# Kernel optimization log

Hardware: AMD Instinct MI355X
Metric: run time of the kernel (lower is better)

Reference implementation:

```python
import jax, jax.numpy as jnp
import numpy as np

B, C, H, W = 8, 320, 32, 32
HEADS, DHEAD = 8, 40
CTX_LEN, CTX_DIM = 77, 768
FF_INNER = 4 * C
GROUPS = 32
HW = H * W


def setup_inputs() -> dict:
    key = jax.random.key(0)
    ks = jax.random.split(key, 16)
    def nrm(k, shape, s=0.02):
        return (jax.random.normal(k, shape) * s).astype(jnp.float32)
    z = lambda *s: jnp.zeros(s, jnp.float32)
    o = lambda *s: jnp.ones(s, jnp.float32)
    inp = {}
    inp["x"] = jax.random.normal(ks[0], (B, C, H, W), jnp.float32)
    inp["context"] = jax.random.normal(ks[1], (B, CTX_LEN, CTX_DIM), jnp.float32)
    inp["vis_mask"] = jax.random.uniform(ks[2], (B, HW, HW)) > 0.5
    inp["v2t_mask"] = jax.random.uniform(ks[3], (B, HW, CTX_LEN)) > 0.5
    inp["gn_scale"] = o(C); inp["gn_bias"] = z(C)
    inp["proj_in_w"] = nrm(ks[4], (C, C)); inp["proj_in_b"] = z(C)
    inp["n1_s"] = o(C); inp["n1_b"] = z(C)
    inp["wq1"] = nrm(ks[5], (C, C)); inp["wk1"] = nrm(ks[6], (C, C)); inp["wv1"] = nrm(ks[7], (C, C))
    inp["wo1"] = nrm(ks[8], (C, C)); inp["bo1"] = z(C)
    inp["n2_s"] = o(C); inp["n2_b"] = z(C)
    inp["wq2"] = nrm(ks[9], (C, C)); inp["wk2"] = nrm(ks[10], (CTX_DIM, C)); inp["wv2"] = nrm(ks[11], (CTX_DIM, C))
    inp["wo2"] = nrm(ks[12], (C, C)); inp["bo2"] = z(C)
    inp["n3_s"] = o(C); inp["n3_b"] = z(C)
    inp["ff_w1"] = nrm(ks[13], (C, 2 * FF_INNER)); inp["ff_b1"] = z(2 * FF_INNER)
    inp["ff_w2"] = nrm(ks[14], (FF_INNER, C)); inp["ff_b2"] = z(C)
    inp["proj_out_w"] = nrm(ks[15], (C, C)); inp["proj_out_b"] = z(C)
    return inp


def group_norm(x, scale, bias, eps=1e-6):
    b, c, h, w = x.shape
    xg = x.reshape(b, GROUPS, -1)
    mu = xg.mean(-1, keepdims=True)
    var = xg.var(-1, keepdims=True)
    xn = ((xg - mu) * jax.lax.rsqrt(var + eps)).reshape(b, c, h, w)
    return xn * scale[None, :, None, None] + bias[None, :, None, None]


def layer_norm(x, s, b, eps=1e-5):
    mu = x.mean(-1, keepdims=True)
    var = x.var(-1, keepdims=True)
    return (x - mu) * jax.lax.rsqrt(var + eps) * s + b


def mha(xq, ctx, wq, wk, wv, wo, bo, mask):
    # CrossAttention: manual einsum softmax with boolean mask broadcast over heads
    b, n, _ = xq.shape
    m = ctx.shape[1]
    split = lambda t: t.reshape(b, -1, HEADS, DHEAD).transpose(0, 2, 1, 3)
    q = split(xq @ wq)   # [b,h,n,d]
    k = split(ctx @ wk)  # [b,h,m,d]
    v = split(ctx @ wv)
    sim = jnp.einsum('bhid,bhjd->bhij', q, k) * (DHEAD ** -0.5)
    if mask is not None:
        sim = jnp.where(mask[:, None, :, :], sim, jnp.finfo(sim.dtype).min)
    attn = jax.nn.softmax(sim, axis=-1)
    out = jnp.einsum('bhij,bhjd->bhid', attn, v)
    out = out.transpose(0, 2, 1, 3).reshape(b, n, HEADS * DHEAD)
    return out @ wo + bo


def reference(x, context, vis_mask, v2t_mask, gn_scale, gn_bias, proj_in_w, proj_in_b,
              n1_s, n1_b, wq1, wk1, wv1, wo1, bo1,
              n2_s, n2_b, wq2, wk2, wv2, wo2, bo2,
              n3_s, n3_b, ff_w1, ff_b1, ff_w2, ff_b2,
              proj_out_w, proj_out_b):
    x_in = x
    h = group_norm(x, gn_scale, gn_bias)
    # 1x1 conv proj_in == per-pixel linear; flatten b c h w -> b (hw) c
    h = h.reshape(B, C, HW).transpose(0, 2, 1) @ proj_in_w + proj_in_b
    # masked self-attention (vis mask)
    h = h + mha(layer_norm(h, n1_s, n1_b), layer_norm(h, n1_s, n1_b),
                wq1, wk1, wv1, wo1, bo1, vis_mask)
    # masked cross-attention to text (v2t mask)
    h = h + mha(layer_norm(h, n2_s, n2_b), context,
                wq2, wk2, wv2, wo2, bo2, v2t_mask)
    # GEGLU feedforward (glu=True, mult=4)
    y = layer_norm(h, n3_s, n3_b) @ ff_w1 + ff_b1
    a, g = jnp.split(y, 2, axis=-1)
    h = h + (a * jax.nn.gelu(g, approximate=False)) @ ff_w2 + ff_b2
    # proj_out + residual
    out = (h @ proj_out_w + proj_out_b).transpose(0, 2, 1).reshape(B, C, H, W)
    return out + x_in
```

## Files before the change

kernel.cpp:

```cpp
#include <hip/hip_runtime.h>
#include <hip/hip_bf16.h>
#include <math.h>


#define Bsz   8
#define Cch   320
#define HW    1024
#define NTOK  (Bsz*HW)
#define HEADS 8
#define DHEAD 40
#define CTXL  77
#define CTXD  768
#define FFI   1280
#define MCTX  (Bsz*CTXL)
#define MCTXP 640

typedef unsigned short u16;
typedef unsigned long long u64;
typedef __attribute__((ext_vector_type(8))) u16    u16x8;
typedef __attribute__((ext_vector_type(8))) __bf16 bf16x8;
typedef __attribute__((ext_vector_type(4))) float  f32x4;

__device__ inline u16 f2b(float f) {
    unsigned u = __float_as_uint(f);
    return (u16)((u + 0x7FFFu + ((u >> 16) & 1u)) >> 16);
}

__global__ __launch_bounds__(256) void gn_apply(
    const float* __restrict__ x, const float* __restrict__ gnA,
    const float* __restrict__ gnB, u16* __restrict__ out)
{
    __shared__ u16 T[64*72];
    const int tid = threadIdx.x;
    const int c0 = blockIdx.x * 64;
    const int p0 = blockIdx.y * 64;
    const int b  = blockIdx.z;
    for (int e = tid; e < 512; e += 256) {
        int r = e >> 3, ch = e & 7;
        const float* src = x + ((size_t)(b*Cch + c0 + r))*HW + p0 + ch*8;
        float a  = gnA[b*Cch + c0 + r];
        float bb = gnB[b*Cch + c0 + r];
        float4 v0 = *(const float4*)src;
        float4 v1 = *(const float4*)(src + 4);
        u16x8 val;
        val[0] = f2b(v0.x*a + bb); val[1] = f2b(v0.y*a + bb);
        val[2] = f2b(v0.z*a + bb); val[3] = f2b(v0.w*a + bb);
        val[4] = f2b(v1.x*a + bb); val[5] = f2b(v1.y*a + bb);
        val[6] = f2b(v1.z*a + bb); val[7] = f2b(v1.w*a + bb);
        *(u16x8*)&T[r*72 + (ch ^ (r & 7))*8] = val;
    }
    __syncthreads();
    for (int e = tid; e < 4096; e += 256) {
        int p = e >> 6, c = e & 63;
        u16 v = T[c*72 + (((p >> 3) ^ (c & 7))*8) + (p & 7)];
        out[((size_t)(b*HW + p0 + p))*Cch + c0 + c] = v;
    }
}

__global__ __launch_bounds__(256) void layernorm_kernel(
    const float* __restrict__ in, const float* __restrict__ s,
    const float* __restrict__ bgain, u16* __restrict__ out)
{
    int t = blockIdx.x*4 + (threadIdx.x >> 6);
    int lane = threadIdx.x & 63;
    const float* row = in + (size_t)t*Cch;
    float v[5];
    float sum = 0.f, sq = 0.f;
    #pragma unroll
    for (int i = 0; i < 5; ++i) {
        v[i] = row[lane + 64*i];
        sum += v[i]; sq += v[i]*v[i];
    }
    #pragma unroll
    for (int off = 32; off > 0; off >>= 1) {
        sum += __shfl_xor(sum, off);
        sq  += __shfl_xor(sq,  off);
    }
    float mean = sum * (1.f/320.f);
    float var  = sq  * (1.f/320.f) - mean*mean;
    float inv  = rsqrtf(var + 1e-5f);
    u16* orow = out + (size_t)t*Cch;
    #pragma unroll
    for (int i = 0; i < 5; ++i) {
        int c = lane + 64*i;
        orow[c] = f2b((v[i]-mean)*inv*s[c] + bgain[c]);
    }
}

struct WDesc { const float* src; u16* dst; int K; int N; int tiles; float scl; };
struct WPack { WDesc w[12]; };

#define WT_TILES 620
#define CTXBLK   240

__global__ __launch_bounds__(256) void preamble(
    WPack p, const float* __restrict__ ctxsrc, u16* __restrict__ ctxdst,
    const void* __restrict__ vis, const void* __restrict__ v2t,
    u64* __restrict__ bvis, u64* __restrict__ bv2t,
    const float* __restrict__ x, const float* __restrict__ gscale,
    const float* __restrict__ gbias, float* __restrict__ gnA,
    float* __restrict__ gnB)
{
    __shared__ u16 T[64*72];
    int blk = blockIdx.x;
    int tid = threadIdx.x;
    if (blk < WT_TILES) {
        int t = blk;
        #pragma unroll
        for (int i = 0; i < 12; ++i) {
            int nt = p.w[i].tiles;
            if (t < nt) {
                const int K = p.w[i].K, N = p.w[i].N;
                const int ntN = N >> 6;
                const int tk = t / ntN, tn = t - tk*ntN;
                const float scl = p.w[i].scl;
                const float* src = p.w[i].src;
                u16* dst = p.w[i].dst;
                for (int e = tid; e < 512; e += 256) {
                    int r = e >> 3, ch = e & 7;
                    const float* sp = src + (size_t)(tk*64 + r)*N + tn*64 + ch*8;
                    float4 v0 = *(const float4*)sp;
                    float4 v1 = *(const float4*)(sp + 4);
                    u16x8 val;
                    val[0] = f2b(v0.x*scl); val[1] = f2b(v0.y*scl);
                    val[2] = f2b(v0.z*scl); val[3] = f2b(v0.w*scl);
                    val[4] = f2b(v1.x*scl); val[5] = f2b(v1.y*scl);
                    val[6] = f2b(v1.z*scl); val[7] = f2b(v1.w*scl);
                    *(u16x8*)&T[r*72 + (ch ^ (r & 7))*8] = val;
                }
                __syncthreads();
                for (int e = tid; e < 4096; e += 256) {
                    int n = e >> 6, k = e & 63;
                    u16 v = T[k*72 + (((n >> 3) ^ (k & 7))*8) + (n & 7)];
                    dst[(size_t)(tn*64 + n)*K + tk*64 + k] = v;
                }
                return;
            }
            t -= nt;
        }
        return;
    }
    if (blk < WT_TILES + CTXBLK) {
        int idx = (blk - WT_TILES)*2048 + tid*8;
        int r = idx / CTXD;
        u16x8 val = {};
        if (r < MCTX) {
            float4 v0 = *(const float4*)(ctxsrc + idx);
            float4 v1 = *(const float4*)(ctxsrc + idx + 4);
            val[0] = f2b(v0.x); val[1] = f2b(v0.y);
            val[2] = f2b(v0.z); val[3] = f2b(v0.w);
            val[4] = f2b(v1.x); val[5] = f2b(v1.y);
            val[6] = f2b(v1.z); val[7] = f2b(v1.w);
        }
        *(u16x8*)(ctxdst + idx) = val;
        return;
    }
    if (blk >= WT_TILES + CTXBLK + 4096) {
        int gb = blk - (WT_TILES + CTXBLK + 4096);
        int b = gb >> 5, g = gb & 31;
        __shared__ float rs[256], rq[256];
        const float4* xg = (const float4*)(x + ((size_t)b*Cch + g*10)*HW);
        float s = 0.f, q = 0.f;
        #pragma unroll
        for (int i = 0; i < 10; ++i) {
            float4 v = xg[tid + i*256];
            s += v.x + v.y + v.z + v.w;
            q += v.x*v.x + v.y*v.y + v.z*v.z + v.w*v.w;
        }
        rs[tid] = s; rq[tid] = q; __syncthreads();
        for (int off = 128; off > 0; off >>= 1) {
            if (tid < off) { rs[tid] += rs[tid+off]; rq[tid] += rq[tid+off]; }
            __syncthreads();
        }
        if (tid < 10) {
            float mean = rs[0] * (1.f/10240.f);
            float var  = rq[0] * (1.f/10240.f) - mean*mean;
            float inv  = rsqrtf(var + 1e-6f);
            int chn = g*10 + tid;
            float a = inv * gscale[chn];
            gnA[b*Cch + chn] = a;
            gnB[b*Cch + chn] = gbias[chn] - mean*a;
        }
        return;
    }
    __shared__ int any;
    if (tid == 0) any = 0;
    __syncthreads();
    const unsigned char* probe = (const unsigned char*)vis;
    for (int i = tid; i < 4096; i += 256)
        if ((i & 3) && probe[i]) any = 1;
    __syncthreads();
    const int isU8 = any;
    int mb = blk - WT_TILES - CTXBLK;
    const void* mask; u64* bits; int Lkv, nw;
    if (mb < 2048) { mask = vis; bits = bvis; Lkv = HW;   nw = 16; }
    else           { mask = v2t; bits = bv2t; Lkv = CTXL; nw = 2; mb -= 2048; }
    const int wv = tid >> 6, lane = tid & 63;
    const int row = mb*4 + wv;
    const unsigned char* m8  = (const unsigned char*)mask;
    const int*           m32 = (const int*)mask;
    const size_t base = (size_t)row * Lkv;
    for (int w = 0; w < nw; ++w) {
        int j = w*64 + lane;
        bool on = (j < Lkv) && (isU8 ? (m8[base+j] != 0) : (m32[base+j] != 0));
        u64 word = __ballot(on);
        if (lane == 0) bits[(size_t)row*nw + w] = word;
    }
}

__global__ __launch_bounds__(512) void gemm_bf16(
    const u16* __restrict__ A, const u16* __restrict__ Wt,
    const float* __restrict__ bias, const float* __restrict__ res,
    float* __restrict__ out, u16* __restrict__ out_bf, int M, int N, int K)
{
    __shared__ u16 As[2][128*40];
    __shared__ u16 Bs[2][64*40];
    const int tid  = threadIdx.x;
    const int lane = tid & 63;
    const int w    = tid >> 6;
    const int mp   = w >> 1;
    const int np   = w & 1;
    const int m0   = blockIdx.y * 128;
    const int n0   = blockIdx.x * 64;
    const int fr   = lane & 15, fg = lane >> 4;
    const int ar   = tid >> 2, ac = tid & 3;
    const bool hasB = tid < 256;

    const u16* pa = A  + (size_t)(m0 + ar)*K + ac*8;
    const u16* pb = Wt + (size_t)(n0 + ar)*K + ac*8;
    const int nk = K >> 5;

    *(u16x8*)&As[0][ar*40 + ac*8] = *(const u16x8*)pa;
    if (hasB) *(u16x8*)&Bs[0][ar*40 + ac*8] = *(const u16x8*)pb;
    u16x8 xa = *(const u16x8*)(pa + 32);
    u16x8 ya = *(const u16x8*)(pa + 64);
    u16x8 xb = {}, yb = {};
    if (hasB) { xb = *(const u16x8*)(pb + 32); yb = *(const u16x8*)(pb + 64); }

    f32x4 acc[2][2] = {};
    for (int i = 0; i < nk; i += 2) {
        __syncthreads();
        *(u16x8*)&As[1][ar*40 + ac*8] = xa;
        if (hasB) *(u16x8*)&Bs[1][ar*40 + ac*8] = xb;
        if (i + 3 < nk) {
            xa = *(const u16x8*)(pa + 32*(i+3));
            if (hasB) xb = *(const u16x8*)(pb + 32*(i+3));
        }
        {
            bf16x8 a0 = *(const bf16x8*)&As[0][(mp*32      + fr)*40 + fg*8];
            bf16x8 a1 = *(const bf16x8*)&As[0][(mp*32 + 16 + fr)*40 + fg*8];
            #pragma unroll
            for (int t = 0; t < 2; ++t) {
                bf16x8 b = *(const bf16x8*)&Bs[0][((np*2+t)*16 + fr)*40 + fg*8];
                acc[0][t] = __builtin_amdgcn_mfma_f32_16x16x32_bf16(a0, b, acc[0][t], 0, 0, 0);
                acc[1][t] = __builtin_amdgcn_mfma_f32_16x16x32_bf16(a1, b, acc[1][t], 0, 0, 0);
            }
        }
        __syncthreads();
        if (i + 2 < nk) {
            *(u16x8*)&As[0][ar*40 + ac*8] = ya;
            if (hasB) *(u16x8*)&Bs[0][ar*40 + ac*8] = yb;
            if (i + 4 < nk) {
                ya = *(const u16x8*)(pa + 32*(i+4));
                if (hasB) yb = *(const u16x8*)(pb + 32*(i+4));
            }
        }
        {
            bf16x8 a0 = *(const bf16x8*)&As[1][(mp*32      + fr)*40 + fg*8];
            bf16x8 a1 = *(const bf16x8*)&As[1][(mp*32 + 16 + fr)*40 + fg*8];
            #pragma unroll
            for (int t = 0; t < 2; ++t) {
                bf16x8 b = *(const bf16x8*)&Bs[1][((np*2+t)*16 + fr)*40 + fg*8];
                acc[0][t] = __builtin_amdgcn_mfma_f32_16x16x32_bf16(a0, b, acc[0][t], 0, 0, 0);
                acc[1][t] = __builtin_amdgcn_mfma_f32_16x16x32_bf16(a1, b, acc[1][t], 0, 0, 0);
            }
        }
    }
    #pragma unroll
    for (int at = 0; at < 2; ++at) {
        #pragma unroll
        for (int t = 0; t < 2; ++t) {
            int gn = n0 + (np*2+t)*16 + fr;
            float bv = bias ? bias[gn] : 0.f;
            #pragma unroll
            for (int i = 0; i < 4; ++i) {
                int gm = m0 + mp*32 + at*16 + fg*4 + i;
                float v = acc[at][t][i] + bv;
                if (res) v += res[(size_t)gm*N + gn];
                if (out) out[(size_t)gm*N + gn] = v;
                if (out_bf) out_bf[(size_t)gm*N + gn] = f2b(v);
            }
        }
    }
}

__global__ __launch_bounds__(512) void gemm_pout(
    const u16* __restrict__ A, const u16* __restrict__ Wt,
    const float* __restrict__ bias, const float* __restrict__ x,
    float* __restrict__ out, int K)
{
    __shared__ u16 As[2][128*40];
    __shared__ u16 Bs[2][64*40];
    const int tid  = threadIdx.x;
    const int lane = tid & 63;
    const int w    = tid >> 6;
    const int mp   = w >> 1;
    const int np   = w & 1;
    const int m0   = blockIdx.y * 128;
    const int n0   = blockIdx.x * 64;
    const int fr   = lane & 15, fg = lane >> 4;
    const int ar   = tid >> 2, ac = tid & 3;
    const bool hasB = tid < 256;

    const u16* pa = A  + (size_t)(m0 + ar)*K + ac*8;
    const u16* pb = Wt + (size_t)(n0 + ar)*K + ac*8;
    const int nk = K >> 5;

    *(u16x8*)&As[0][ar*40 + ac*8] = *(const u16x8*)pa;
    if (hasB) *(u16x8*)&Bs[0][ar*40 + ac*8] = *(const u16x8*)pb;
    u16x8 xa = *(const u16x8*)(pa + 32);
    u16x8 ya = *(const u16x8*)(pa + 64);
    u16x8 xb = {}, yb = {};
    if (hasB) { xb = *(const u16x8*)(pb + 32); yb = *(const u16x8*)(pb + 64); }

    f32x4 acc[2][2] = {};
    for (int i = 0; i < nk; i += 2) {
        __syncthreads();
        *(u16x8*)&As[1][ar*40 + ac*8] = xa;
        if (hasB) *(u16x8*)&Bs[1][ar*40 + ac*8] = xb;
        if (i + 3 < nk) {
            xa = *(const u16x8*)(pa + 32*(i+3));
            if (hasB) xb = *(const u16x8*)(pb + 32*(i+3));
        }
        {
            bf16x8 a0 = *(const bf16x8*)&As[0][(mp*32      + fr)*40 + fg*8];
            bf16x8 a1 = *(const bf16x8*)&As[0][(mp*32 + 16 + fr)*40 + fg*8];
            #pragma unroll
            for (int t = 0; t < 2; ++t) {
                bf16x8 b = *(const bf16x8*)&Bs[0][((np*2+t)*16 + fr)*40 + fg*8];
                acc[0][t] = __builtin_amdgcn_mfma_f32_16x16x32_bf16(a0, b, acc[0][t], 0, 0, 0);
                acc[1][t] = __builtin_amdgcn_mfma_f32_16x16x32_bf16(a1, b, acc[1][t], 0, 0, 0);
            }
        }
        __syncthreads();
        if (i + 2 < nk) {
            *(u16x8*)&As[0][ar*40 + ac*8] = ya;
            if (hasB) *(u16x8*)&Bs[0][ar*40 + ac*8] = yb;
            if (i + 4 < nk) {
                ya = *(const u16x8*)(pa + 32*(i+4));
                if (hasB) yb = *(const u16x8*)(pb + 32*(i+4));
            }
        }
        {
            bf16x8 a0 = *(const bf16x8*)&As[1][(mp*32      + fr)*40 + fg*8];
            bf16x8 a1 = *(const bf16x8*)&As[1][(mp*32 + 16 + fr)*40 + fg*8];
            #pragma unroll
            for (int t = 0; t < 2; ++t) {
                bf16x8 b = *(const bf16x8*)&Bs[1][((np*2+t)*16 + fr)*40 + fg*8];
                acc[0][t] = __builtin_amdgcn_mfma_f32_16x16x32_bf16(a0, b, acc[0][t], 0, 0, 0);
                acc[1][t] = __builtin_amdgcn_mfma_f32_16x16x32_bf16(a1, b, acc[1][t], 0, 0, 0);
            }
        }
    }
    #pragma unroll
    for (int at = 0; at < 2; ++at) {
        #pragma unroll
        for (int t = 0; t < 2; ++t) {
            int gn = n0 + (np*2+t)*16 + fr;
            float bv = bias[gn];
            int gm0 = m0 + mp*32 + at*16 + fg*4;
            int b   = gm0 >> 10;
            int pcol= gm0 & (HW-1);
            size_t o = ((size_t)(b*Cch + gn))*HW + pcol;
            f32x4 xv = *(const f32x4*)&x[o];
            f32x4 vv;
            #pragma unroll
            for (int i = 0; i < 4; ++i) vv[i] = acc[at][t][i] + bv + xv[i];
            *(f32x4*)&out[o] = vv;
        }
    }
}

__global__ __launch_bounds__(512) void ctx_kv_gemm(
    const u16* __restrict__ ctx, const u16* __restrict__ wk,
    const u16* __restrict__ wv, u16* __restrict__ kout, u16* __restrict__ vout)
{
    __shared__ u16 As[2][64*40];
    __shared__ u16 Bs[2][64*40];
    const int tid  = threadIdx.x;
    const int lane = tid & 63;
    const int w    = tid >> 6;
    const int mg   = w >> 1;
    const int np   = w & 1;
    const int m0   = blockIdx.y * 64;
    const int n0   = blockIdx.x * 64;
    const u16* Wt  = blockIdx.z ? wv : wk;
    u16* outp      = blockIdx.z ? vout : kout;
    const int fr   = lane & 15, fg = lane >> 4;
    const bool isA = tid < 256;
    const int cr   = (tid & 255) >> 2, cc = tid & 3;

    const u16* ps = isA ? ctx + (size_t)(m0 + cr)*CTXD + cc*8
                        : Wt  + (size_t)(n0 + cr)*CTXD + cc*8;
    u16* s0 = isA ? &As[0][cr*40 + cc*8] : &Bs[0][cr*40 + cc*8];
    u16* s1 = isA ? &As[1][cr*40 + cc*8] : &Bs[1][cr*40 + cc*8];
    const int nk = CTXD >> 5;

    *(u16x8*)s0 = *(const u16x8*)ps;
    u16x8 xv = *(const u16x8*)(ps + 32);
    u16x8 yv = *(const u16x8*)(ps + 64);

    f32x4 acc[2] = {};
    for (int i = 0; i < nk; i += 2) {
        __syncthreads();
        *(u16x8*)s1 = xv;
        if (i + 3 < nk) xv = *(const u16x8*)(ps + 32*(i+3));
        {
            bf16x8 a = *(const bf16x8*)&As[0][(mg*16 + fr)*40 + fg*8];
            #pragma unroll
            for (int t = 0; t < 2; ++t) {
                bf16x8 b = *(const bf16x8*)&Bs[0][((np*2+t)*16 + fr)*40 + fg*8];
                acc[t] = __builtin_amdgcn_mfma_f32_16x16x32_bf16(a, b, acc[t], 0, 0, 0);
            }
        }
        __syncthreads();
        if (i + 2 < nk) {
            *(u16x8*)s0 = yv;
            if (i + 4 < nk) yv = *(const u16x8*)(ps + 32*(i+4));
        }
        {
            bf16x8 a = *(const bf16x8*)&As[1][(mg*16 + fr)*40 + fg*8];
            #pragma unroll
            for (int t = 0; t < 2; ++t) {
                bf16x8 b = *(const bf16x8*)&Bs[1][((np*2+t)*16 + fr)*40 + fg*8];
                acc[t] = __builtin_amdgcn_mfma_f32_16x16x32_bf16(a, b, acc[t], 0, 0, 0);
            }
        }
    }
    #pragma unroll
    for (int t = 0; t < 2; ++t) {
        int gn = n0 + (np*2+t)*16 + fr;
        #pragma unroll
        for (int i = 0; i < 4; ++i) {
            int gm = m0 + mg*16 + fg*4 + i;
            if (gm < MCTX)
                outp[(size_t)gm*Cch + gn] = f2b(acc[t][i]);
        }
    }
}

__global__ __launch_bounds__(256) void geglu_bf16(
    const u16* __restrict__ A, const u16* __restrict__ Wt,
    const float* __restrict__ b1, u16* __restrict__ out, int M, int K)
{
    __shared__ u16 As[2][128*40];
    __shared__ u16 Ba[2][64*40];
    __shared__ u16 Bg[2][64*40];
    const int tid  = threadIdx.x;
    const int lane = tid & 63;
    const int w    = tid >> 6;
    const int m0   = blockIdx.y * 128;
    const int n0   = blockIdx.x * 64;
    const int fr   = lane & 15, fg = lane >> 4;
    const int ar   = tid >> 2, ac = tid & 3;

    const u16* pa0 = A  + (size_t)(m0 + ar)*K      + ac*8;
    const u16* pa1 = A  + (size_t)(m0 + ar + 64)*K + ac*8;
    const u16* pba = Wt + (size_t)(n0 + ar)*K       + ac*8;
    const u16* pbg = Wt + (size_t)(FFI + n0 + ar)*K + ac*8;
    const int nk = K >> 5;

    *(u16x8*)&As[0][ar*40 + ac*8]      = *(const u16x8*)pa0;
    *(u16x8*)&As[0][(ar+64)*40 + ac*8] = *(const u16x8*)pa1;
    *(u16x8*)&Ba[0][ar*40 + ac*8]      = *(const u16x8*)pba;
    *(u16x8*)&Bg[0][ar*40 + ac*8]      = *(const u16x8*)pbg;
    u16x8 xa0 = *(const u16x8*)(pa0 + 32);
    u16x8 xa1 = *(const u16x8*)(pa1 + 32);
    u16x8 xba = *(const u16x8*)(pba + 32);
    u16x8 xbg = *(const u16x8*)(pbg + 32);
    u16x8 ya0 = *(const u16x8*)(pa0 + 64);
    u16x8 ya1 = *(const u16x8*)(pa1 + 64);
    u16x8 yba = *(const u16x8*)(pba + 64);
    u16x8 ybg = *(const u16x8*)(pbg + 64);

    f32x4 aca[2][4] = {}, acg[2][4] = {};
    for (int i = 0; i < nk; i += 2) {
        __syncthreads();
        *(u16x8*)&As[1][ar*40 + ac*8]      = xa0;
        *(u16x8*)&As[1][(ar+64)*40 + ac*8] = xa1;
        *(u16x8*)&Ba[1][ar*40 + ac*8]      = xba;
        *(u16x8*)&Bg[1][ar*40 + ac*8]      = xbg;
        if (i + 3 < nk) {
            xa0 = *(const u16x8*)(pa0 + 32*(i+3));
            xa1 = *(const u16x8*)(pa1 + 32*(i+3));
            xba = *(const u16x8*)(pba + 32*(i+3));
            xbg = *(const u16x8*)(pbg + 32*(i+3));
        }
        {
            bf16x8 a0 = *(const bf16x8*)&As[0][(w*32      + fr)*40 + fg*8];
            bf16x8 a1 = *(const bf16x8*)&As[0][(w*32 + 16 + fr)*40 + fg*8];
            #pragma unroll
            for (int nt = 0; nt < 4; ++nt) {
                bf16x8 ba = *(const bf16x8*)&Ba[0][(nt*16 + fr)*40 + fg*8];
                bf16x8 bg = *(const bf16x8*)&Bg[0][(nt*16 + fr)*40 + fg*8];
                aca[0][nt] = __builtin_amdgcn_mfma_f32_16x16x32_bf16(a0, ba, aca[0][nt], 0, 0, 0);
                aca[1][nt] = __builtin_amdgcn_mfma_f32_16x16x32_bf16(a1, ba, aca[1][nt], 0, 0, 0);
                acg[0][nt] = __builtin_amdgcn_mfma_f32_16x16x32_bf16(a0, bg, acg[0][nt], 0, 0, 0);
                acg[1][nt] = __builtin_amdgcn_mfma_f32_16x16x32_bf16(a1, bg, acg[1][nt], 0, 0, 0);
            }
        }
        __syncthreads();
        if (i + 2 < nk) {
            *(u16x8*)&As[0][ar*40 + ac*8]      = ya0;
            *(u16x8*)&As[0][(ar+64)*40 + ac*8] = ya1;
            *(u16x8*)&Ba[0][ar*40 + ac*8]      = yba;
            *(u16x8*)&Bg[0][ar*40 + ac*8]      = ybg;
            if (i + 4 < nk) {
                ya0 = *(const u16x8*)(pa0 + 32*(i+4));
                ya1 = *(const u16x8*)(pa1 + 32*(i+4));
                yba = *(const u16x8*)(pba + 32*(i+4));
                ybg = *(const u16x8*)(pbg + 32*(i+4));
            }
        }
        {
            bf16x8 a0 = *(const bf16x8*)&As[1][(w*32      + fr)*40 + fg*8];
            bf16x8 a1 = *(const bf16x8*)&As[1][(w*32 + 16 + fr)*40 + fg*8];
            #pragma unroll
            for (int nt = 0; nt < 4; ++nt) {
                bf16x8 ba = *(const bf16x8*)&Ba[1][(nt*16 + fr)*40 + fg*8];
                bf16x8 bg = *(const bf16x8*)&Bg[1][(nt*16 + fr)*40 + fg*8];
                aca[0][nt] = __builtin_amdgcn_mfma_f32_16x16x32_bf16(a0, ba, aca[0][nt], 0, 0, 0);
                aca[1][nt] = __builtin_amdgcn_mfma_f32_16x16x32_bf16(a1, ba, aca[1][nt], 0, 0, 0);
                acg[0][nt] = __builtin_amdgcn_mfma_f32_16x16x32_bf16(a0, bg, acg[0][nt], 0, 0, 0);
                acg[1][nt] = __builtin_amdgcn_mfma_f32_16x16x32_bf16(a1, bg, acg[1][nt], 0, 0, 0);
            }
        }
    }
    #pragma unroll
    for (int at = 0; at < 2; ++at) {
        #pragma unroll
        for (int nt = 0; nt < 4; ++nt) {
            int gn = n0 + nt*16 + fr;
            float ba = b1[gn], bg = b1[FFI + gn];
            #pragma unroll
            for (int i = 0; i < 4; ++i) {
                int gm = m0 + w*32 + at*16 + fg*4 + i;
                float av = aca[at][nt][i] + ba;
                float gv = acg[at][nt][i] + bg;
                float gel = 0.5f*gv*(1.f + erff(gv*0.70710678118654752f));
                out[(size_t)gm*FFI + gn] = f2b(av*gel);
            }
        }
    }
}

__global__ __launch_bounds__(256) void transpose_v(
    const u16* __restrict__ in, int istride, u16* __restrict__ out,
    int Ltok, int ostride)
{
    __shared__ u16 T[64*72];
    const int tid = threadIdx.x;
    const int c0 = blockIdx.x * 64;
    const int t0 = blockIdx.y * 64;
    const int b  = blockIdx.z;
    for (int e = tid; e < 512; e += 256) {
        int r = e >> 3, ch = e & 7;
        u16x8 val = {};
        if (t0 + r < Ltok)
            val = *(const u16x8*)(in + ((size_t)(b*Ltok + t0 + r))*istride + c0 + ch*8);
        *(u16x8*)&T[r*72 + (ch ^ (r & 7))*8] = val;
    }
    __syncthreads();
    for (int e = tid; e < 4096; e += 256) {
        int c = e >> 6, t = e & 63;
        u16 v = T[t*72 + (((c >> 3) ^ (t & 7))*8) + (c & 7)];
        out[((size_t)(b*Cch + c0 + c))*ostride + t0 + t] = v;
    }
}

__global__ __launch_bounds__(256) void flash_mfma(
    const u16* __restrict__ qb, int qstride,
    const u16* __restrict__ kb, int kstride,
    const u16* __restrict__ vt, int vstride,
    const u64* __restrict__ mbits, int nw,
    u16* __restrict__ out,
    int Lkv)
{
    __shared__ u16 QPs[64*72];
    __shared__ u16 Ks[64*72];
    __shared__ u16 Vs[48*72];

    const int tid  = threadIdx.x;
    const int lane = tid & 63;
    const int w    = tid >> 6;
    const int col  = lane & 15;
    const int quad = lane >> 4;
    const int q0   = blockIdx.x * 64;
    const int h    = blockIdx.y;
    const int b    = blockIdx.z;
    const int ch   = tid & 7;
    const int r0   = tid >> 3;

    {
        const u16* qT = qb + ((size_t)(b*HW + q0))*qstride + (size_t)h*DHEAD + ch*8;
        u16x8 v0 = {}, v1 = {};
        if (ch < 5) {
            v0 = *(const u16x8*)(qT + (size_t)r0*qstride);
            v1 = *(const u16x8*)(qT + (size_t)(r0+32)*qstride);
        }
        *(u16x8*)&QPs[r0*72 + ch*8]      = v0;
        *(u16x8*)&QPs[(r0+32)*72 + ch*8] = v1;
    }
    __syncthreads();
    const bf16x8 qa0 = *(const bf16x8*)&QPs[(w*16 + col)*72 +  0 + quad*8];
    const bf16x8 qa1 = *(const bf16x8*)&QPs[(w*16 + col)*72 + 32 + quad*8];

    const bool kok = ch < 5;
    const u16* kR0 = kb + (size_t)b*Lkv*kstride + (size_t)h*DHEAD + ch*8
                        + (size_t)r0*kstride;
    const u16* kR1 = kR0 + (size_t)32*kstride;
    const int d1   = 32 + (tid >> 3);
    const u16* vR0 = vt + ((size_t)(b*Cch + h*DHEAD))*vstride + ch*8
                        + (size_t)r0*vstride;
    const u16* vR1 = vt + ((size_t)(b*Cch + h*DHEAD))*vstride + ch*8
                        + (size_t)d1*vstride;
    const u64* mrow = mbits + ((size_t)(b*HW + q0 + w*16 + quad*4))*nw;

    f32x4 acc_o[3] = {};

    const int nkt = (Lkv + 63) / 64;
    for (int jt = 0; jt < nkt; ++jt) {
        const int j0 = jt*64;
        __syncthreads();
        {
            u16x8 v0 = {}, v1 = {};
            if (kok && (j0 + r0      < Lkv)) v0 = *(const u16x8*)kR0;
            if (kok && (j0 + r0 + 32 < Lkv)) v1 = *(const u16x8*)kR1;
            *(u16x8*)&Ks[r0*72 + ch*8]      = v0;
            *(u16x8*)&Ks[(r0+32)*72 + ch*8] = v1;
        }
        {
            u16x8 v0 = {};
            if (r0 < DHEAD) v0 = *(const u16x8*)vR0;
            *(u16x8*)&Vs[r0*72 + ch*8] = v0;
            if (tid < 128) {
                u16x8 v1 = {};
                if (d1 < DHEAD) v1 = *(const u16x8*)vR1;
                else if (d1 == DHEAD) {
                    #pragma unroll
                    for (int z = 0; z < 8; ++z) v1[z] = 0x3F80;
                }
                *(u16x8*)&Vs[d1*72 + ch*8] = v1;
            }
        }
        __syncthreads();

        u64 mw[4];
        #pragma unroll
        for (int i = 0; i < 4; ++i) mw[i] = mrow[i*nw + jt];

        f32x4 s[4] = {};
        #pragma unroll
        for (int nt = 0; nt < 4; ++nt) {
            bf16x8 b0 = *(const bf16x8*)&Ks[(nt*16 + col)*72 +  0 + quad*8];
            bf16x8 b1 = *(const bf16x8*)&Ks[(nt*16 + col)*72 + 32 + quad*8];
            s[nt] = __builtin_amdgcn_mfma_f32_16x16x32_bf16(qa0, b0, s[nt], 0, 0, 0);
            s[nt] = __builtin_amdgcn_mfma_f32_16x16x32_bf16(qa1, b1, s[nt], 0, 0, 0);
        }

        #pragma unroll
        for (int i = 0; i < 4; ++i) {
            #pragma unroll
            for (int nt = 0; nt < 4; ++nt) {
                float p = __builtin_amdgcn_exp2f(s[nt][i]);
                unsigned bits = (unsigned)(mw[i] >> (nt*16));
                s[nt][i] = ((bits >> col) & 1u) ? p : 0.f;
            }
        }

        #pragma unroll
        for (int nt = 0; nt < 4; ++nt)
            #pragma unroll
            for (int i = 0; i < 4; ++i)
                QPs[(w*16 + quad*4 + i)*68 + nt*16 + col] =
                    (u16)(__float_as_uint(s[nt][i]) >> 16);

        bf16x8 pa0, pa1;
        __builtin_memcpy(&pa0, &QPs[(w*16 + col)*68 +  0 + quad*8], 16);
        __builtin_memcpy(&pa1, &QPs[(w*16 + col)*68 + 32 + quad*8], 16);
        #pragma unroll
        for (int nt = 0; nt < 3; ++nt) {
            bf16x8 vb0 = *(const bf16x8*)&Vs[(nt*16 + col)*72 +  0 + quad*8];
            bf16x8 vb1 = *(const bf16x8*)&Vs[(nt*16 + col)*72 + 32 + quad*8];
            acc_o[nt] = __builtin_amdgcn_mfma_f32_16x16x32_bf16(pa0, vb0, acc_o[nt], 0, 0, 0);
            acc_o[nt] = __builtin_amdgcn_mfma_f32_16x16x32_bf16(pa1, vb1, acc_o[nt], 0, 0, 0);
        }

        kR0 += (size_t)64*kstride;
        kR1 += (size_t)64*kstride;
        vR0 += 64;
        vR1 += 64;
    }

    float inv_l[4];
    #pragma unroll
    for (int i = 0; i < 4; ++i)
        inv_l[i] = 1.f / __shfl(acc_o[2][i], (lane & 48) | 8);

    #pragma unroll
    for (int nt = 0; nt < 3; ++nt) {
        int d = nt*16 + col;
        if (d < DHEAD) {
            #pragma unroll
            for (int i = 0; i < 4; ++i) {
                int q = q0 + w*16 + quad*4 + i;
                out[((size_t)(b*HW + q))*Cch + h*DHEAD + d] = f2b(acc_o[nt][i] * inv_l[i]);
            }
        }
    }
}

extern "C" void kernel_launch(void* const* d_in, const int* in_sizes, int n_in,
                              void* d_out, int out_size, void* d_ws, size_t ws_size,
                              hipStream_t stream)
{
    const float* x        = (const float*)d_in[0];
    const float* context  = (const float*)d_in[1];
    const void*  vis_mask = d_in[2];
    const void*  v2t_mask = d_in[3];
    const float* gn_s     = (const float*)d_in[4];
    const float* gn_b     = (const float*)d_in[5];
    const float* proj_in_w= (const float*)d_in[6];
    const float* proj_in_b= (const float*)d_in[7];
    const float* n1_s     = (const float*)d_in[8];
    const float* n1_b     = (const float*)d_in[9];
    const float* wq1      = (const float*)d_in[10];
    const float* wk1      = (const float*)d_in[11];
    const float* wv1      = (const float*)d_in[12];
    const float* wo1      = (const float*)d_in[13];
    const float* bo1      = (const float*)d_in[14];
    const float* n2_s     = (const float*)d_in[15];
    const float* n2_b     = (const float*)d_in[16];
    const float* wq2      = (const float*)d_in[17];
    const float* wk2      = (const float*)d_in[18];
    const float* wv2      = (const float*)d_in[19];
    const float* wo2      = (const float*)d_in[20];
    const float* bo2      = (const float*)d_in[21];
    const float* n3_s     = (const float*)d_in[22];
    const float* n3_b     = (const float*)d_in[23];
    const float* ff_w1    = (const float*)d_in[24];
    const float* ff_b1    = (const float*)d_in[25];
    const float* ff_w2    = (const float*)d_in[26];
    const float* ff_b2    = (const float*)d_in[27];
    const float* pout_w   = (const float*)d_in[28];
    const float* pout_b   = (const float*)d_in[29];
    float* out = (float*)d_out;

    const size_t TOKC = (size_t)NTOK*Cch;
    float* ws   = (float*)d_ws;
    float* Hb   = ws;
    u16*   QKV  = (u16*)(Hb + TOKC);
    u16*   Vt_g = QKV + 3*TOKC;
    u16*   G_bf = QKV;
    u16*   T0b  = Vt_g + TOKC;
    u16*   T1b  = T0b + TOKC;
    u16*   Hb_bf= T1b + TOKC;
    u16*   Wbf  = Hb_bf + TOKC;
    u64*   mb_vis = (u64*)(Wbf + 2539520);
    u64*   mb_v2t = mb_vis + 131072;
    u16*   ctx_bf = (u16*)(mb_v2t + 16384);
    u16*   Kc_bf  = ctx_bf + MCTXP*CTXD;
    u16*   Vc_bf  = Kc_bf + 640*Cch;
    float* gnA    = (float*)(Vc_bf + 640*Cch);
    float* gnB    = gnA + Bsz*Cch;

    u16* w_q1  = Wbf;
    u16* w_k1  = Wbf +  102400;
    u16* w_v1  = Wbf +  204800;
    u16* w_pin = Wbf +  307200;
    u16* w_o1  = Wbf +  409600;
    u16* w_q2  = Wbf +  512000;
    u16* w_o2  = Wbf +  614400;
    u16* w_ff1 = Wbf +  716800;
    u16* w_ff2 = Wbf + 1536000;
    u16* w_po  = Wbf + 1945600;
    u16* w_k2  = Wbf + 2048000;
    u16* w_v2  = Wbf + 2293760;

    const float qscale = 0.15811388300841897f * 1.4426950408889634f;
    WPack pack;
    pack.w[0]  = { wq1,       w_q1,  Cch, Cch, 25,  qscale };
    pack.w[1]  = { wk1,       w_k1,  Cch, Cch, 25,  1.f };
    pack.w[2]  = { wv1,       w_v1,  Cch, Cch, 25,  1.f };
    pack.w[3]  = { proj_in_w, w_pin, Cch, Cch, 25,  1.f };
    pack.w[4]  = { wo1,       w_o1,  Cch, Cch, 25,  1.f };
    pack.w[5]  = { wq2,       w_q2,  Cch, Cch, 25,  qscale };
    pack.w[6]  = { wo2,       w_o2,  Cch, Cch, 25,  1.f };
    pack.w[7]  = { ff_w1,     w_ff1, Cch, 2*FFI, 200, 1.f };
    pack.w[8]  = { ff_w2,     w_ff2, FFI, Cch, 100, 1.f };
    pack.w[9]  = { pout_w,    w_po,  Cch, Cch, 25,  1.f };
    pack.w[10] = { wk2,       w_k2,  CTXD, Cch, 60, 1.f };
    pack.w[11] = { wv2,       w_v2,  CTXD, Cch, 60, 1.f };

    dim3 blk256(256);
    dim3 blk512(512);
    dim3 gTok(Cch/64, NTOK/128);
    dim3 gQKV(960/64, NTOK/128);
    dim3 gKV(Cch/64, MCTXP/64, 2);
    dim3 gFF(FFI/64, NTOK/128);
    dim3 gFA(HW/64, HEADS, Bsz);
    dim3 gTrS(Cch/64, HW/64, Bsz);
    dim3 gTrX(Cch/64, 2, Bsz);
    dim3 gGN(Cch/64, HW/64, Bsz);

    preamble<<<WT_TILES + CTXBLK + 4096 + 256, blk256, 0, stream>>>(
        pack, context, ctx_bf, vis_mask, v2t_mask, mb_vis, mb_v2t,
        x, gn_s, gn_b, gnA, gnB);

    gn_apply<<<gGN, blk256, 0, stream>>>(x, gnA, gnB, T0b);
    gemm_bf16<<<gTok, blk512, 0, stream>>>(T0b, w_pin, proj_in_b, nullptr, Hb, nullptr, NTOK, Cch, Cch);

    layernorm_kernel<<<NTOK/4, blk256, 0, stream>>>(Hb, n1_s, n1_b, T0b);
    gemm_bf16<<<gQKV, blk512, 0, stream>>>(T0b, w_q1, nullptr, nullptr, nullptr, QKV, NTOK, 960, Cch);
    transpose_v<<<gTrS, blk256, 0, stream>>>(QKV + 640, 960, Vt_g, HW, HW);
    flash_mfma<<<gFA, blk256, 0, stream>>>(QKV, 960, QKV + 320, 960, Vt_g, HW,
                                           mb_vis, 16, T1b, HW);
    gemm_bf16<<<gTok, blk512, 0, stream>>>(T1b, w_o1, bo1, Hb, Hb, nullptr, NTOK, Cch, Cch);

    layernorm_kernel<<<NTOK/4, blk256, 0, stream>>>(Hb, n2_s, n2_b, T0b);
    gemm_bf16<<<gTok, blk512, 0, stream>>>(T0b, w_q2, nullptr, nullptr, nullptr, QKV, NTOK, Cch, Cch);
    ctx_kv_gemm<<<gKV, blk512, 0, stream>>>(ctx_bf, w_k2, w_v2, Kc_bf, Vc_bf);
    transpose_v<<<gTrX, blk256, 0, stream>>>(Vc_bf, Cch, Vt_g, CTXL, 128);
    flash_mfma<<<gFA, blk256, 0, stream>>>(QKV, Cch, Kc_bf, Cch, Vt_g, 128,
                                           mb_v2t, 2, T1b, CTXL);
    gemm_bf16<<<gTok, blk512, 0, stream>>>(T1b, w_o2, bo2, Hb, Hb, nullptr, NTOK, Cch, Cch);

    layernorm_kernel<<<NTOK/4, blk256, 0, stream>>>(Hb, n3_s, n3_b, T0b);
    geglu_bf16<<<gFF, blk256, 0, stream>>>(T0b, w_ff1, ff_b1, G_bf, NTOK, Cch);
    gemm_bf16<<<gTok, blk512, 0, stream>>>(G_bf, w_ff2, ff_b2, Hb, nullptr, Hb_bf, NTOK, Cch, FFI);

    gemm_pout<<<gTok, blk512, 0, stream>>>(Hb_bf, w_po, pout_b, x, out, Cch);
}
```

Before: 387.9 us.

## Widen GEGLU kernel to 512 threads and prefetch K/V tiles in flash attention

The GEGLU GEMM now launches 512 threads per block. Each thread loads one A row chunk and one B row chunk, and the 8 waves are split into a 4x2 grid over M and N, so each wave holds half as many accumulators. The flash attention kernel now register-prefetches the next K/V tile from global memory while computing the current one, and writes the constant ones/zero rows of the V tile once instead of every iteration. The aim is more waves in flight and global-load latency hidden behind MFMA work. The cost is extra register pressure for the prefetch buffers, and the V-padding rows rely on staying untouched across iterations.

```diff
diff --git a/kernel.cpp b/kernel.cpp
--- a/kernel.cpp
+++ b/kernel.cpp
@@ -449,7 +449,7 @@
     }
 }
 
-__global__ __launch_bounds__(256) void geglu_bf16(
+__global__ __launch_bounds__(512) void geglu_bf16(
     const u16* __restrict__ A, const u16* __restrict__ Wt,
     const float* __restrict__ b1, u16* __restrict__ out, int M, int K)
 {
@@ -459,94 +459,83 @@
     const int tid  = threadIdx.x;
     const int lane = tid & 63;
     const int w    = tid >> 6;
+    const int mp   = w >> 1;
+    const int np   = w & 1;
     const int m0   = blockIdx.y * 128;
     const int n0   = blockIdx.x * 64;
     const int fr   = lane & 15, fg = lane >> 4;
     const int ar   = tid >> 2, ac = tid & 3;
-
-    const u16* pa0 = A  + (size_t)(m0 + ar)*K      + ac*8;
-    const u16* pa1 = A  + (size_t)(m0 + ar + 64)*K + ac*8;
-    const u16* pba = Wt + (size_t)(n0 + ar)*K       + ac*8;
-    const u16* pbg = Wt + (size_t)(FFI + n0 + ar)*K + ac*8;
-    const int nk = K >> 5;
-
-    *(u16x8*)&As[0][ar*40 + ac*8]      = *(const u16x8*)pa0;
-    *(u16x8*)&As[0][(ar+64)*40 + ac*8] = *(const u16x8*)pa1;
-    *(u16x8*)&Ba[0][ar*40 + ac*8]      = *(const u16x8*)pba;
-    *(u16x8*)&Bg[0][ar*40 + ac*8]      = *(const u16x8*)pbg;
-    u16x8 xa0 = *(const u16x8*)(pa0 + 32);
-    u16x8 xa1 = *(const u16x8*)(pa1 + 32);
-    u16x8 xba = *(const u16x8*)(pba + 32);
-    u16x8 xbg = *(const u16x8*)(pbg + 32);
-    u16x8 ya0 = *(const u16x8*)(pa0 + 64);
-    u16x8 ya1 = *(const u16x8*)(pa1 + 64);
-    u16x8 yba = *(const u16x8*)(pba + 64);
-    u16x8 ybg = *(const u16x8*)(pbg + 64);
-
-    f32x4 aca[2][4] = {}, acg[2][4] = {};
+    const int nk   = K >> 5;
+
+    const u16* pa = A + (size_t)(m0 + ar)*K + ac*8;
+    const int bq = (ar < 64) ? (n0 + ar) : (FFI + n0 + ar - 64);
+    const u16* pb = Wt + (size_t)bq*K + ac*8;
+    u16* bs0 = (ar < 64) ? &Ba[0][ar*40 + ac*8] : &Bg[0][(ar-64)*40 + ac*8];
+    u16* bs1 = (ar < 64) ? &Ba[1][ar*40 + ac*8] : &Bg[1][(ar-64)*40 + ac*8];
+
+    *(u16x8*)&As[0][ar*40 + ac*8] = *(const u16x8*)pa;
+    *(u16x8*)bs0 = *(const u16x8*)pb;
+    u16x8 xa = *(const u16x8*)(pa + 32);
+    u16x8 xb = *(const u16x8*)(pb + 32);
+    u16x8 ya = *(const u16x8*)(pa + 64);
+    u16x8 yb = *(const u16x8*)(pb + 64);
+
+    f32x4 aca[2][2] = {}, acg[2][2] = {};
     for (int i = 0; i < nk; i += 2) {
         __syncthreads();
-        *(u16x8*)&As[1][ar*40 + ac*8]      = xa0;
-        *(u16x8*)&As[1][(ar+64)*40 + ac*8] = xa1;
-        *(u16x8*)&Ba[1][ar*40 + ac*8]      = xba;
-        *(u16x8*)&Bg[1][ar*40 + ac*8]      = xbg;
+        *(u16x8*)&As[1][ar*40 + ac*8] = xa;
+        *(u16x8*)bs1 = xb;
         if (i + 3 < nk) {
-            xa0 = *(const u16x8*)(pa0 + 32*(i+3));
-            xa1 = *(const u16x8*)(pa1 + 32*(i+3));
-            xba = *(const u16x8*)(pba + 32*(i+3));
-            xbg = *(const u16x8*)(pbg + 32*(i+3));
+            xa = *(const u16x8*)(pa + 32*(i+3));
+            xb = *(const u16x8*)(pb + 32*(i+3));
         }
         {
-            bf16x8 a0 = *(const bf16x8*)&As[0][(w*32      + fr)*40 + fg*8];
-            bf16x8 a1 = *(const bf16x8*)&As[0][(w*32 + 16 + fr)*40 + fg*8];
-            #pragma unroll
-            for (int nt = 0; nt < 4; ++nt) {
-                bf16x8 ba = *(const bf16x8*)&Ba[0][(nt*16 + fr)*40 + fg*8];
-                bf16x8 bg = *(const bf16x8*)&Bg[0][(nt*16 + fr)*40 + fg*8];
-                aca[0][nt] = __builtin_amdgcn_mfma_f32_16x16x32_bf16(a0, ba, aca[0][nt], 0, 0, 0);
-                aca[1][nt] = __builtin_amdgcn_mfma_f32_16x16x32_bf16(a1, ba, aca[1][nt], 0, 0, 0);
-                acg[0][nt] = __builtin_amdgcn_mfma_f32_16x16x32_bf16(a0, bg, acg[0][nt], 0, 0, 0);
-                acg[1][nt] = __builtin_amdgcn_mfma_f32_16x16x32_bf16(a1, bg, acg[1][nt], 0, 0, 0);
+            bf16x8 a0 = *(const bf16x8*)&As[0][(mp*32      + fr)*40 + fg*8];
+            bf16x8 a1 = *(const bf16x8*)&As[0][(mp*32 + 16 + fr)*40 + fg*8];
+            #pragma unroll
+            for (int t = 0; t < 2; ++t) {
+                bf16x8 ba = *(const bf16x8*)&Ba[0][((np*2+t)*16 + fr)*40 + fg*8];
+                bf16x8 bg = *(const bf16x8*)&Bg[0][((np*2+t)*16 + fr)*40 + fg*8];
+                aca[0][t] = __builtin_amdgcn_mfma_f32_16x16x32_bf16(a0, ba, aca[0][t], 0, 0, 0);
+                aca[1][t] = __builtin_amdgcn_mfma_f32_16x16x32_bf16(a1, ba, aca[1][t], 0, 0, 0);
+                acg[0][t] = __builtin_amdgcn_mfma_f32_16x16x32_bf16(a0, bg, acg[0][t], 0, 0, 0);
+                acg[1][t] = __builtin_amdgcn_mfma_f32_16x16x32_bf16(a1, bg, acg[1][t], 0, 0, 0);
             }
         }
         __syncthreads();
         if (i + 2 < nk) {
-            *(u16x8*)&As[0][ar*40 + ac*8]      = ya0;
-            *(u16x8*)&As[0][(ar+64)*40 + ac*8] = ya1;
-            *(u16x8*)&Ba[0][ar*40 + ac*8]      = yba;
-            *(u16x8*)&Bg[0][ar*40 + ac*8]      = ybg;
+            *(u16x8*)&As[0][ar*40 + ac*8] = ya;
+            *(u16x8*)bs0 = yb;
             if (i + 4 < nk) {
-                ya0 = *(const u16x8*)(pa0 + 32*(i+4));
-                ya1 = *(const u16x8*)(pa1 + 32*(i+4));
-                yba = *(const u16x8*)(pba + 32*(i+4));
-                ybg = *(const u16x8*)(pbg + 32*(i+4));
+                ya = *(const u16x8*)(pa + 32*(i+4));
+                yb = *(const u16x8*)(pb + 32*(i+4));
             }
         }
         {
-            bf16x8 a0 = *(const bf16x8*)&As[1][(w*32      + fr)*40 + fg*8];
-            bf16x8 a1 = *(const bf16x8*)&As[1][(w*32 + 16 + fr)*40 + fg*8];
-            #pragma unroll
-            for (int nt = 0; nt < 4; ++nt) {
-                bf16x8 ba = *(const bf16x8*)&Ba[1][(nt*16 + fr)*40 + fg*8];
-                bf16x8 bg = *(const bf16x8*)&Bg[1][(nt*16 + fr)*40 + fg*8];
-                aca[0][nt] = __builtin_amdgcn_mfma_f32_16x16x32_bf16(a0, ba, aca[0][nt], 0, 0, 0);
-                aca[1][nt] = __builtin_amdgcn_mfma_f32_16x16x32_bf16(a1, ba, aca[1][nt], 0, 0, 0);
-                acg[0][nt] = __builtin_amdgcn_mfma_f32_16x16x32_bf16(a0, bg, acg[0][nt], 0, 0, 0);
-                acg[1][nt] = __builtin_amdgcn_mfma_f32_16x16x32_bf16(a1, bg, acg[1][nt], 0, 0, 0);
+            bf16x8 a0 = *(const bf16x8*)&As[1][(mp*32      + fr)*40 + fg*8];
+            bf16x8 a1 = *(const bf16x8*)&As[1][(mp*32 + 16 + fr)*40 + fg*8];
+            #pragma unroll
+            for (int t = 0; t < 2; ++t) {
+                bf16x8 ba = *(const bf16x8*)&Ba[1][((np*2+t)*16 + fr)*40 + fg*8];
+                bf16x8 bg = *(const bf16x8*)&Bg[1][((np*2+t)*16 + fr)*40 + fg*8];
+                aca[0][t] = __builtin_amdgcn_mfma_f32_16x16x32_bf16(a0, ba, aca[0][t], 0, 0, 0);
+                aca[1][t] = __builtin_amdgcn_mfma_f32_16x16x32_bf16(a1, ba, aca[1][t], 0, 0, 0);
+                acg[0][t] = __builtin_amdgcn_mfma_f32_16x16x32_bf16(a0, bg, acg[0][t], 0, 0, 0);
+                acg[1][t] = __builtin_amdgcn_mfma_f32_16x16x32_bf16(a1, bg, acg[1][t], 0, 0, 0);
             }
         }
     }
     #pragma unroll
     for (int at = 0; at < 2; ++at) {
         #pragma unroll
-        for (int nt = 0; nt < 4; ++nt) {
-            int gn = n0 + nt*16 + fr;
+        for (int t = 0; t < 2; ++t) {
+            int gn = n0 + (np*2+t)*16 + fr;
             float ba = b1[gn], bg = b1[FFI + gn];
             #pragma unroll
             for (int i = 0; i < 4; ++i) {
-                int gm = m0 + w*32 + at*16 + fg*4 + i;
-                float av = aca[at][nt][i] + ba;
-                float gv = acg[at][nt][i] + bg;
+                int gm = m0 + mp*32 + at*16 + fg*4 + i;
+                float av = aca[at][t][i] + ba;
+                float gv = acg[at][t][i] + bg;
                 float gel = 0.5f*gv*(1.f + erff(gv*0.70710678118654752f));
                 out[(size_t)gm*FFI + gn] = f2b(av*gel);
             }
@@ -611,9 +600,15 @@
         *(u16x8*)&QPs[r0*72 + ch*8]      = v0;
         *(u16x8*)&QPs[(r0+32)*72 + ch*8] = v1;
     }
-    __syncthreads();
-    const bf16x8 qa0 = *(const bf16x8*)&QPs[(w*16 + col)*72 +  0 + quad*8];
-    const bf16x8 qa1 = *(const bf16x8*)&QPs[(w*16 + col)*72 + 32 + quad*8];
+    if (tid >= 64 && tid < 128) {
+        int dc = 32 + (tid >> 3);
+        u16x8 v = {};
+        if (dc == DHEAD) {
+            #pragma unroll
+            for (int z = 0; z < 8; ++z) v[z] = 0x3F80;
+        }
+        *(u16x8*)&Vs[dc*72 + ch*8] = v;
+    }
 
     const bool kok = ch < 5;
     const u16* kR0 = kb + (size_t)b*Lkv*kstride + (size_t)h*DHEAD + ch*8
@@ -625,33 +620,37 @@
     const u16* vR1 = vt + ((size_t)(b*Cch + h*DHEAD))*vstride + ch*8
                         + (size_t)d1*vstride;
     const u64* mrow = mbits + ((size_t)(b*HW + q0 + w*16 + quad*4))*nw;
+    const bool vok1 = tid < 64;
+
+    u16x8 nk0 = {}, nk1 = {}, nv0, nv1 = {};
+    if (kok && (r0      < Lkv)) nk0 = *(const u16x8*)kR0;
+    if (kok && (r0 + 32 < Lkv)) nk1 = *(const u16x8*)kR1;
+    nv0 = *(const u16x8*)vR0;
+    if (vok1) nv1 = *(const u16x8*)vR1;
+
+    __syncthreads();
+    const bf16x8 qa0 = *(const bf16x8*)&QPs[(w*16 + col)*72 +  0 + quad*8];
+    const bf16x8 qa1 = *(const bf16x8*)&QPs[(w*16 + col)*72 + 32 + quad*8];
 
     f32x4 acc_o[3] = {};
 
     const int nkt = (Lkv + 63) / 64;
     for (int jt = 0; jt < nkt; ++jt) {
-        const int j0 = jt*64;
-        __syncthreads();
-        {
-            u16x8 v0 = {}, v1 = {};
-            if (kok && (j0 + r0      < Lkv)) v0 = *(const u16x8*)kR0;
-            if (kok && (j0 + r0 + 32 < Lkv)) v1 = *(const u16x8*)kR1;
-            *(u16x8*)&Ks[r0*72 + ch*8]      = v0;
-            *(u16x8*)&Ks[(r0+32)*72 + ch*8] = v1;
-        }
-        {
-            u16x8 v0 = {};
-            if (r0 < DHEAD) v0 = *(const u16x8*)vR0;
-            *(u16x8*)&Vs[r0*72 + ch*8] = v0;
-            if (tid < 128) {
-                u16x8 v1 = {};
-                if (d1 < DHEAD) v1 = *(const u16x8*)vR1;
-                else if (d1 == DHEAD) {
-                    #pragma unroll
-                    for (int z = 0; z < 8; ++z) v1[z] = 0x3F80;
-                }
-                *(u16x8*)&Vs[d1*72 + ch*8] = v1;
-            }
+        __syncthreads();
+        *(u16x8*)&Ks[r0*72 + ch*8]      = nk0;
+        *(u16x8*)&Ks[(r0+32)*72 + ch*8] = nk1;
+        *(u16x8*)&Vs[r0*72 + ch*8]      = nv0;
+        if (vok1) *(u16x8*)&Vs[d1*72 + ch*8] = nv1;
+        if (jt + 1 < nkt) {
+            const int j0n = (jt + 1)*64;
+            kR0 += (size_t)64*kstride;
+            kR1 += (size_t)64*kstride;
+            vR0 += 64; vR1 += 64;
+            nk0 = (u16x8){}; nk1 = (u16x8){};
+            if (kok && (j0n + r0      < Lkv)) nk0 = *(const u16x8*)kR0;
+            if (kok && (j0n + r0 + 32 < Lkv)) nk1 = *(const u16x8*)kR1;
+            nv0 = *(const u16x8*)vR0;
+            if (vok1) nv1 = *(const u16x8*)vR1;
         }
         __syncthreads();
 
@@ -695,11 +694,6 @@
             acc_o[nt] = __builtin_amdgcn_mfma_f32_16x16x32_bf16(pa0, vb0, acc_o[nt], 0, 0, 0);
             acc_o[nt] = __builtin_amdgcn_mfma_f32_16x16x32_bf16(pa1, vb1, acc_o[nt], 0, 0, 0);
         }
-
-        kR0 += (size_t)64*kstride;
-        kR1 += (size_t)64*kstride;
-        vR0 += 64;
-        vR1 += 64;
     }
 
     float inv_l[4];
@@ -836,7 +830,7 @@
     gemm_bf16<<<gTok, blk512, 0, stream>>>(T1b, w_o2, bo2, Hb, Hb, nullptr, NTOK, Cch, Cch);
 
     layernorm_kernel<<<NTOK/4, blk256, 0, stream>>>(Hb, n3_s, n3_b, T0b);
-    geglu_bf16<<<gFF, blk256, 0, stream>>>(T0b, w_ff1, ff_b1, G_bf, NTOK, Cch);
+    geglu_bf16<<<gFF, blk512, 0, stream>>>(T0b, w_ff1, ff_b1, G_bf, NTOK, Cch);
     gemm_bf16<<<gTok, blk512, 0, stream>>>(G_bf, w_ff2, ff_b2, Hb, nullptr, Hb_bf, NTOK, Cch, FFI);
 
     gemm_pout<<<gTok, blk512, 0, stream>>>(Hb_bf, w_po, pout_b, x, out, Cch);
```

Measured after the change: 377.8 us. 2.6% less time.
